# Performance work log

Hardware: AMD Instinct MI355X
Metric: run time of the kernel (lower is better)

## Reference

```python
import jax, jax.numpy as jnp
import numpy as np

D_MODEL = 32
D_STATE = 16
D_CONV = 4
D_INNER = 64  # expand * d_model
DT_RANK = 2   # ceil(d_model / 16)


def silu(x):
    return x * jax.nn.sigmoid(x)


def _mamba_params(key, scale=0.05):
    ks = jax.random.split(key, 7)
    p = {}
    p['in_w'] = jax.random.normal(ks[0], (2 * D_INNER, D_MODEL), jnp.float32) * scale
    p['conv_w'] = jax.random.normal(ks[1], (D_INNER, 1, D_CONV), jnp.float32) * scale
    p['conv_b'] = jax.random.normal(ks[2], (D_INNER,), jnp.float32) * scale
    p['xproj_w'] = jax.random.normal(ks[3], (DT_RANK + 2 * D_STATE, D_INNER), jnp.float32) * scale
    p['dt_w'] = jax.random.normal(ks[4], (D_INNER, DT_RANK), jnp.float32) * scale
    p['dt_b'] = jax.random.normal(ks[5], (D_INNER,), jnp.float32) * scale
    # S4D-real init: A = [1..d_state] broadcast over d_inner
    p['A_log'] = jnp.log(jnp.broadcast_to(jnp.arange(1, D_STATE + 1, dtype=jnp.float32), (D_INNER, D_STATE)))
    p['D'] = jnp.ones((D_INNER,), jnp.float32)
    p['out_w'] = jax.random.normal(ks[6], (D_MODEL, D_INNER), jnp.float32) * scale
    return p


def mamba(x, in_w, conv_w, conv_b, xproj_w, dt_w, dt_b, A_log, Dp, out_w):
    # x: (B, L, d_model)
    Bsz, L, _ = x.shape
    xz = x @ in_w.T                                   # (B, L, 2*d_inner)
    xi, z = jnp.split(xz, 2, axis=-1)
    # causal depthwise conv over L
    xc = jnp.pad(xi.transpose(0, 2, 1), ((0, 0), (0, 0), (D_CONV - 1, 0)))  # (B, d_inner, L+3)
    xc = jax.lax.conv_general_dilated(xc, conv_w, (1,), 'VALID',
                                      dimension_numbers=('NCH', 'OIH', 'NCH'),
                                      feature_group_count=D_INNER)
    xi = silu(xc.transpose(0, 2, 1) + conv_b)          # (B, L, d_inner)
    dbc = xi @ xproj_w.T                               # (B, L, dt_rank + 2*d_state)
    dt = dbc[..., :DT_RANK]
    Bm = dbc[..., DT_RANK:DT_RANK + D_STATE]           # (B, L, d_state)
    Cm = dbc[..., DT_RANK + D_STATE:]                  # (B, L, d_state)
    delta = jax.nn.softplus(dt @ dt_w.T + dt_b)        # (B, L, d_inner)
    A = -jnp.exp(A_log)                                # (d_inner, d_state)
    deltaA = jnp.exp(delta[..., None] * A)             # (B, L, d_inner, d_state)
    deltaBx = delta[..., None] * Bm[:, :, None, :] * xi[..., None]

    def step(h, t):
        dA, dBx = t
        h = dA * h + dBx
        return h, h

    h0 = jnp.zeros((Bsz, D_INNER, D_STATE), x.dtype)
    _, hs = jax.lax.scan(step, h0, (deltaA.transpose(1, 0, 2, 3), deltaBx.transpose(1, 0, 2, 3)))
    hs = hs.transpose(1, 0, 2, 3)                      # (B, L, d_inner, d_state)
    y = jnp.einsum('blds,bls->bld', hs, Cm) + Dp * xi
    y = y * silu(z)
    return y @ out_w.T                                 # (B, L, d_model)


def setup_inputs() -> dict:
    key = jax.random.key(0)
    ks = jax.random.split(key, 12)
    s = 0.05
    inp = {'inputs': jax.random.normal(ks[0], (32, 512, 64, 64), jnp.float32)}
    inp['proj_avg_w'] = jax.random.normal(ks[1], (D_MODEL, 1), jnp.float32) * s
    inp['proj_avg_b'] = jax.random.normal(ks[2], (D_MODEL,), jnp.float32) * s
    inp['proj_max_w'] = jax.random.normal(ks[3], (D_MODEL, 1), jnp.float32) * s
    inp['proj_max_b'] = jax.random.normal(ks[4], (D_MODEL,), jnp.float32) * s
    inp['gate_w'] = jax.random.normal(ks[5], (1, 2), jnp.float32) * s
    inp['gate_b'] = jax.random.normal(ks[6], (1,), jnp.float32) * s
    inp['out_w'] = jax.random.normal(ks[7], (1, D_MODEL), jnp.float32) * s
    inp['out_b'] = jax.random.normal(ks[8], (1,), jnp.float32) * s
    pf = _mamba_params(ks[9])
    pb = _mamba_params(ks[10])
    for k, v in pf.items():
        inp['f_' + k] = v
    for k, v in pb.items():
        inp['b_' + k] = v
    return inp


def reference(inputs, proj_avg_w, proj_avg_b, proj_max_w, proj_max_b, gate_w, gate_b,
              out_w, out_b,
              f_in_w, f_conv_w, f_conv_b, f_xproj_w, f_dt_w, f_dt_b, f_A_log, f_D, f_out_w,
              b_in_w, b_conv_w, b_conv_b, b_xproj_w, b_dt_w, b_dt_b, b_A_log, b_D, b_out_w):
    # global avg / max pool -> (B, C, 1)
    x_avg = jnp.mean(inputs, axis=(2, 3))[..., None]
    x_max = jnp.max(inputs, axis=(2, 3))[..., None]
    gate_in = jnp.concatenate([x_avg, x_max], axis=-1)            # (B, C, 2)
    alpha = jax.nn.sigmoid(gate_in @ gate_w.T + gate_b)           # (B, C, 1)
    xa = x_avg @ proj_avg_w.T + proj_avg_b                        # (B, C, d_model)
    xm = x_max @ proj_max_w.T + proj_max_b
    fwd = (f_in_w, f_conv_w, f_conv_b, f_xproj_w, f_dt_w, f_dt_b, f_A_log, f_D, f_out_w)
    bwd = (b_in_w, b_conv_w, b_conv_b, b_xproj_w, b_dt_w, b_dt_b, b_A_log, b_D, b_out_w)
    y_avg = mamba(xa, *fwd) + jnp.flip(mamba(jnp.flip(xa, 1), *bwd), 1)
    y_max = mamba(xm, *fwd) + jnp.flip(mamba(jnp.flip(xm, 1), *bwd), 1)
    y = alpha * y_avg + (1.0 - alpha) * y_max
    att = jax.nn.sigmoid(y @ out_w.T + out_b)                     # (B, C, 1)
    return att[..., None]                                         # (B, C, 1, 1)
```

## Files before the change

### kernel.cpp

```cpp
#include <hip/hip_runtime.h>
#include <math.h>

#define OFF_YPART 32768
#define OFF_PD    294912
#define OFF_PX    (OFF_PD + 4194304)
#define OFF_PG    (OFF_PX + 4194304)
#define OFF_BCB   (OFF_PG + 4194304)
#define OFF_BCC   (OFF_BCB + 524288)
#define OFF_YB    (OFF_BCC + 524288)

__global__ __launch_bounds__(256) void kreduce(const float* __restrict__ in,
                                               float* __restrict__ xavg,
                                               float* __restrict__ xmax) {
    const int bl = blockIdx.x;
    const float* p = in + (size_t)bl * 4096;
    const int t = threadIdx.x;
    float s = 0.f, m = -INFINITY;
#pragma unroll
    for (int it = 0; it < 4; ++it) {
        float4 v = *reinterpret_cast<const float4*>(p + (size_t)(it * 256 + t) * 4);
        s += v.x + v.y + v.z + v.w;
        m = fmaxf(m, fmaxf(fmaxf(v.x, v.y), fmaxf(v.z, v.w)));
    }
#pragma unroll
    for (int o = 1; o < 64; o <<= 1) {
        s += __shfl_xor(s, o);
        m = fmaxf(m, __shfl_xor(m, o));
    }
    __shared__ float ls[4], lm[4];
    const int w = t >> 6;
    if ((t & 63) == 0) { ls[w] = s; lm[w] = m; }
    __syncthreads();
    if (t == 0) {
        s = ls[0] + ls[1] + ls[2] + ls[3];
        m = fmaxf(fmaxf(lm[0], lm[1]), fmaxf(lm[2], lm[3]));
        xavg[bl] = s * (1.f / 4096.f);
        xmax[bl] = m;
    }
}

__device__ __forceinline__ int dbc_slot(int j) {
    return j < 2 ? j : (j < 18 ? 2 * j - 2 : 2 * j - 33);
}

__global__ __launch_bounds__(512) void kprep(
    const float* __restrict__ xavg, const float* __restrict__ xmax,
    float* __restrict__ ws,
    const float* __restrict__ paw, const float* __restrict__ pab,
    const float* __restrict__ pmw, const float* __restrict__ pmb,
    const float* __restrict__ outw_outer,
    const float* __restrict__ f_in_w, const float* __restrict__ f_conv_w,
    const float* __restrict__ f_conv_b, const float* __restrict__ f_xproj_w,
    const float* __restrict__ f_dt_w, const float* __restrict__ f_dt_b,
    const float* __restrict__ f_D, const float* __restrict__ f_out_w,
    const float* __restrict__ b_in_w, const float* __restrict__ b_conv_w,
    const float* __restrict__ b_conv_b, const float* __restrict__ b_xproj_w,
    const float* __restrict__ b_dt_w, const float* __restrict__ b_dt_b,
    const float* __restrict__ b_D, const float* __restrict__ b_out_w)
{
    const int tid = threadIdx.x;
    const int c  = blockIdx.x >> 8;
    const int b  = (blockIdx.x >> 3) & 31;
    const int cq = blockIdx.x & 7;
    const int strm = c >> 1, dir = c & 1;

    const float* in_w = dir ? b_in_w   : f_in_w;
    const float* cwp  = dir ? b_conv_w : f_conv_w;
    const float* cbp  = dir ? b_conv_b : f_conv_b;
    const float* xpw  = dir ? b_xproj_w: f_xproj_w;
    const float* dtwp = dir ? b_dt_w   : f_dt_w;
    const float* dtbp = dir ? b_dt_b   : f_dt_b;
    const float* Dpar = dir ? b_D      : f_D;
    const float* owp  = dir ? b_out_w  : f_out_w;
    const float* projw = strm ? pmw : paw;
    const float* projb = strm ? pmb : pab;
    const float* xin   = strm ? xmax : xavg;

    __shared__ float sseq4[68];
    __shared__ float su[128], sv[128];
    __shared__ float scw[64][4], scb[64], sdtw[64][2], sdtb[64], sD[64], swf[64];
    __shared__ float sxp[34][68];
    __shared__ float sxi[64][68];
    __shared__ float sdbc[64][37];

    if (tid < 67) {
        int g = cq * 64 - 3 + tid;
        float val = 0.f;
        if (g >= 0) val = xin[b * 512 + (dir ? (511 - g) : g)];
        sseq4[tid] = val;
    }
    if (tid < 128) {
        float u = 0.f, v = 0.f;
        const float* row = in_w + tid * 32;
#pragma unroll
        for (int m = 0; m < 32; ++m) {
            u = fmaf(row[m], projw[m], u);
            v = fmaf(row[m], projb[m], v);
        }
        su[tid] = u; sv[tid] = v;
    }
    if (tid < 64) {
#pragma unroll
        for (int k = 0; k < 4; ++k) scw[tid][k] = cwp[tid * 4 + k];
        scb[tid] = cbp[tid];
        sdtw[tid][0] = dtwp[tid * 2];
        sdtw[tid][1] = dtwp[tid * 2 + 1];
        sdtb[tid] = dtbp[tid];
        sD[tid] = Dpar[tid];
        float wf = 0.f;
#pragma unroll
        for (int m = 0; m < 32; ++m) wf = fmaf(outw_outer[m], owp[m * 64 + tid], wf);
        swf[tid] = wf;
    }
    for (int i = tid; i < 34 * 64; i += 512) sxp[i >> 6][i & 63] = xpw[i];
    __syncthreads();

    const int ll8 = tid >> 3;
    const int j8  = tid & 7;
    const int gi  = cq * 64 + ll8;

    {
        float t0 = sseq4[ll8], t1 = sseq4[ll8 + 1], t2 = sseq4[ll8 + 2], t3 = sseq4[ll8 + 3];
        float vv0 = (gi >= 3) ? 1.f : 0.f;
        float vv1 = (gi >= 2) ? 1.f : 0.f;
        float vv2 = (gi >= 1) ? 1.f : 0.f;
#pragma unroll
        for (int k = 0; k < 8; ++k) {
            int di = j8 * 8 + k;
            float u = su[di], v = sv[di];
            float xc = scw[di][0] * fmaf(t0, u, vv0 * v)
                     + scw[di][1] * fmaf(t1, u, vv1 * v)
                     + scw[di][2] * fmaf(t2, u, vv2 * v)
                     + scw[di][3] * fmaf(t3, u, v);
            xc += scb[di];
            float sig = 1.f / (1.f + __expf(-xc));
            sxi[ll8][di] = xc * sig;
        }
    }
    __syncthreads();

    {
        float a0 = 0.f, a1 = 0.f, a2 = 0.f, a3 = 0.f, a4 = 0.f;
        const float4* xr4 = reinterpret_cast<const float4*>(&sxi[ll8][0]);
        const float4* r0 = reinterpret_cast<const float4*>(&sxp[j8 + 0][0]);
        const float4* r1 = reinterpret_cast<const float4*>(&sxp[j8 + 8][0]);
        const float4* r2 = reinterpret_cast<const float4*>(&sxp[j8 + 16][0]);
        const float4* r3 = reinterpret_cast<const float4*>(&sxp[j8 + 24][0]);
        const float4* r4 = (j8 < 2) ? reinterpret_cast<const float4*>(&sxp[j8 + 32][0]) : r0;
        bool extra = (j8 < 2);
#pragma unroll 2
        for (int q = 0; q < 16; ++q) {
            float4 x = xr4[q];
            float4 w;
            w = r0[q]; a0 = fmaf(x.x,w.x,fmaf(x.y,w.y,fmaf(x.z,w.z,fmaf(x.w,w.w,a0))));
            w = r1[q]; a1 = fmaf(x.x,w.x,fmaf(x.y,w.y,fmaf(x.z,w.z,fmaf(x.w,w.w,a1))));
            w = r2[q]; a2 = fmaf(x.x,w.x,fmaf(x.y,w.y,fmaf(x.z,w.z,fmaf(x.w,w.w,a2))));
            w = r3[q]; a3 = fmaf(x.x,w.x,fmaf(x.y,w.y,fmaf(x.z,w.z,fmaf(x.w,w.w,a3))));
            if (extra) { w = r4[q]; a4 = fmaf(x.x,w.x,fmaf(x.y,w.y,fmaf(x.z,w.z,fmaf(x.w,w.w,a4)))); }
        }
        sdbc[ll8][dbc_slot(j8)]      = a0;
        sdbc[ll8][dbc_slot(j8 + 8)]  = a1;
        sdbc[ll8][dbc_slot(j8 + 16)] = a2;
        sdbc[ll8][dbc_slot(j8 + 24)] = a3;
        if (extra) sdbc[ll8][dbc_slot(j8 + 32)] = a4;
    }
    __syncthreads();

    {
        const size_t tile = ((size_t)(c * 32 + b) * 8 + cq) * 4096;
        float dt0 = sdbc[ll8][0], dt1 = sdbc[ll8][1];
        float x3 = sseq4[ll8 + 3];
        float ybp = 0.f;
#pragma unroll 2
        for (int k = 0; k < 8; ++k) {
            int di = j8 * 8 + k;
            float xi = sxi[ll8][di];
            float pre = fmaf(dt0, sdtw[di][0], fmaf(dt1, sdtw[di][1], sdtb[di]));
            float sp = (pre > 20.f) ? pre : __logf(1.f + __expf(pre));
            float zv = fmaf(x3, su[64 + di], sv[64 + di]);
            float g = (zv / (1.f + __expf(-zv))) * swf[di];
            ws[OFF_PD + tile + di * 64 + ll8] = sp;
            ws[OFF_PX + tile + di * 64 + ll8] = sp * xi;
            ws[OFF_PG + tile + di * 64 + ll8] = g;
            ybp = fmaf(g * sD[di], xi, ybp);
        }
        ybp += __shfl_xor(ybp, 1);
        ybp += __shfl_xor(ybp, 2);
        ybp += __shfl_xor(ybp, 4);
        if (j8 == 0) ws[OFF_YB + (size_t)(c * 32 + b) * 512 + gi] = ybp;
    }

    {
        const size_t bb = ((size_t)(c * 32 + b) * 8 + cq) * 1024;
        for (int i = tid; i < 1024; i += 512) {
            int s = i >> 6, t = i & 63;
            ws[OFF_BCB + bb + i] = sdbc[t][2 + 2 * s];
            ws[OFF_BCC + bb + i] = sdbc[t][3 + 2 * s];
        }
    }
}

#define DPP_ADD(v, ctrl) ((v) + __int_as_float(__builtin_amdgcn_update_dpp(0, __float_as_int(v), (ctrl), 0xF, 0xF, true)))

__global__ __launch_bounds__(256) void kscan(
    float* __restrict__ ws,
    const float* __restrict__ f_A_log, const float* __restrict__ b_A_log)
{
    const int tid = threadIdx.x;
    const int c  = blockIdx.x >> 7;
    const int dq = (blockIdx.x >> 5) & 3;
    const int b  = blockIdx.x & 31;
    const int dir = c & 1;
    const float* alog = dir ? b_A_log : f_A_log;

    const int dd = tid >> 4;
    const int s  = tid & 15;
    const int d  = dq * 16 + dd;
    const float cA = -expf(alog[d * 16 + s]) * 1.44269504088896340736f;
    float h = 0.f;

    __shared__ float sd[16][68], sx[16][68], sg[16][68];
    __shared__ float sB[16][68], sC[16][68];
    __shared__ float syT[16][68];
    __shared__ float syb[64];

    const int srow = tid >> 4;
    const int scol = (tid & 15) * 4;
    float* ypart = ws + OFF_YPART;
    const size_t cb512 = (size_t)(c * 32 + b) * 512;

    {
        const size_t tb = (size_t)(c * 32 + b) * 8;
        *reinterpret_cast<float4*>(&sd[srow][scol]) =
            *reinterpret_cast<const float4*>(ws + OFF_PD + tb * 4096 + dq * 1024 + srow * 64 + scol);
        *reinterpret_cast<float4*>(&sx[srow][scol]) =
            *reinterpret_cast<const float4*>(ws + OFF_PX + tb * 4096 + dq * 1024 + srow * 64 + scol);
        *reinterpret_cast<float4*>(&sg[srow][scol]) =
            *reinterpret_cast<const float4*>(ws + OFF_PG + tb * 4096 + dq * 1024 + srow * 64 + scol);
        *reinterpret_cast<float4*>(&sB[srow][scol]) =
            *reinterpret_cast<const float4*>(ws + OFF_BCB + tb * 1024 + srow * 64 + scol);
        *reinterpret_cast<float4*>(&sC[srow][scol]) =
            *reinterpret_cast<const float4*>(ws + OFF_BCC + tb * 1024 + srow * 64 + scol);
        if (dq == 0 && tid < 64) syb[tid] = ws[OFF_YB + cb512 + tid];
    }
    __syncthreads();

    for (int chunk = 0; chunk < 8; ++chunk) {
        float4 nd, nx, ng, nB, nC;
        float nyb = 0.f;
        const bool pf = (chunk < 7);
        if (pf) {
            const size_t tb1 = (size_t)(c * 32 + b) * 8 + chunk + 1;
            nd = *reinterpret_cast<const float4*>(ws + OFF_PD + tb1 * 4096 + dq * 1024 + srow * 64 + scol);
            nx = *reinterpret_cast<const float4*>(ws + OFF_PX + tb1 * 4096 + dq * 1024 + srow * 64 + scol);
            ng = *reinterpret_cast<const float4*>(ws + OFF_PG + tb1 * 4096 + dq * 1024 + srow * 64 + scol);
            nB = *reinterpret_cast<const float4*>(ws + OFF_BCB + tb1 * 1024 + srow * 64 + scol);
            nC = *reinterpret_cast<const float4*>(ws + OFF_BCC + tb1 * 1024 + srow * 64 + scol);
            if (dq == 0 && tid < 64) nyb = ws[OFF_YB + cb512 + (chunk + 1) * 64 + tid];
        }

        {
#pragma unroll 2
            for (int m = 0; m < 16; ++m) {
                float4 de = *reinterpret_cast<const float4*>(&sd[dd][4 * m]);
                float4 dx = *reinterpret_cast<const float4*>(&sx[dd][4 * m]);
                float4 gq = *reinterpret_cast<const float4*>(&sg[dd][4 * m]);
                float4 Bq = *reinterpret_cast<const float4*>(&sB[s][4 * m]);
                float4 Cq = *reinterpret_cast<const float4*>(&sC[s][4 * m]);
                float4 val;
                float a, pc;
                a = exp2f(de.x * cA); h = fmaf(a, h, dx.x * Bq.x); pc = h * Cq.x;
                pc = DPP_ADD(pc, 0x101); pc = DPP_ADD(pc, 0x102);
                pc = DPP_ADD(pc, 0x104); pc = DPP_ADD(pc, 0x108);
                val.x = pc * gq.x;
                a = exp2f(de.y * cA); h = fmaf(a, h, dx.y * Bq.y); pc = h * Cq.y;
                pc = DPP_ADD(pc, 0x101); pc = DPP_ADD(pc, 0x102);
                pc = DPP_ADD(pc, 0x104); pc = DPP_ADD(pc, 0x108);
                val.y = pc * gq.y;
                a = exp2f(de.z * cA); h = fmaf(a, h, dx.z * Bq.z); pc = h * Cq.z;
                pc = DPP_ADD(pc, 0x101); pc = DPP_ADD(pc, 0x102);
                pc = DPP_ADD(pc, 0x104); pc = DPP_ADD(pc, 0x108);
                val.z = pc * gq.z;
                a = exp2f(de.w * cA); h = fmaf(a, h, dx.w * Bq.w); pc = h * Cq.w;
                pc = DPP_ADD(pc, 0x101); pc = DPP_ADD(pc, 0x102);
                pc = DPP_ADD(pc, 0x104); pc = DPP_ADD(pc, 0x108);
                val.w = pc * gq.w;
                if (s == 0) *reinterpret_cast<float4*>(&syT[dd][4 * m]) = val;
            }
        }
        __syncthreads();

        {
            const int tt4 = tid >> 2;
            const int j4  = tid & 3;
            float acc = syT[j4 * 4][tt4] + syT[j4 * 4 + 1][tt4]
                      + syT[j4 * 4 + 2][tt4] + syT[j4 * 4 + 3][tt4];
            acc += __shfl_xor(acc, 1);
            acc += __shfl_xor(acc, 2);
            if (j4 == 0) {
                int i = chunk * 64 + tt4;
                int l = dir ? (511 - i) : i;
                float res = acc + (dq == 0 ? syb[tt4] : 0.f);
                ypart[((c * 4 + dq) * 32 + b) * 512 + l] = res;
            }
        }
        __syncthreads();

        if (pf) {
            *reinterpret_cast<float4*>(&sd[srow][scol]) = nd;
            *reinterpret_cast<float4*>(&sx[srow][scol]) = nx;
            *reinterpret_cast<float4*>(&sg[srow][scol]) = ng;
            *reinterpret_cast<float4*>(&sB[srow][scol]) = nB;
            *reinterpret_cast<float4*>(&sC[srow][scol]) = nC;
            if (dq == 0 && tid < 64) syb[tid] = nyb;
            __syncthreads();
        }
    }
}

__global__ __launch_bounds__(256) void kfinal(const float* __restrict__ xavg,
                                              const float* __restrict__ xmax,
                                              const float* __restrict__ ypart,
                                              const float* __restrict__ gate_w,
                                              const float* __restrict__ gate_b,
                                              const float* __restrict__ out_b,
                                              float* __restrict__ out) {
    const int idx = blockIdx.x * 256 + threadIdx.x;
    float xa = xavg[idx], xm = xmax[idx];
    float alpha = 1.f / (1.f + __expf(-(fmaf(xa, gate_w[0], fmaf(xm, gate_w[1], gate_b[0])))));
    float sa = 0.f, sm = 0.f;
#pragma unroll
    for (int k = 0; k < 8; ++k)  sa += ypart[k * 16384 + idx];
#pragma unroll
    for (int k = 8; k < 16; ++k) sm += ypart[k * 16384 + idx];
    float y = alpha * sa + (1.f - alpha) * sm + out_b[0];
    out[idx] = 1.f / (1.f + __expf(-y));
}

extern "C" void kernel_launch(void* const* d_in, const int* in_sizes, int n_in,
                              void* d_out, int out_size, void* d_ws, size_t ws_size,
                              hipStream_t stream) {
    const float* inp = (const float*)d_in[0];
    const float* paw = (const float*)d_in[1];
    const float* pab = (const float*)d_in[2];
    const float* pmw = (const float*)d_in[3];
    const float* pmb = (const float*)d_in[4];
    const float* gw  = (const float*)d_in[5];
    const float* gb  = (const float*)d_in[6];
    const float* ow  = (const float*)d_in[7];
    const float* ob  = (const float*)d_in[8];

    float* ws = (float*)d_ws;
    float* xavg = ws;
    float* xmax = ws + 16384;
    float* ypart = ws + OFF_YPART;
    float* out = (float*)d_out;

    kreduce<<<16384, 256, 0, stream>>>(inp, xavg, xmax);
    kprep<<<1024, 512, 0, stream>>>(
        xavg, xmax, ws, paw, pab, pmw, pmb, ow,
        (const float*)d_in[9],  (const float*)d_in[10], (const float*)d_in[11], (const float*)d_in[12],
        (const float*)d_in[13], (const float*)d_in[14], (const float*)d_in[16], (const float*)d_in[17],
        (const float*)d_in[18], (const float*)d_in[19], (const float*)d_in[20], (const float*)d_in[21],
        (const float*)d_in[22], (const float*)d_in[23], (const float*)d_in[25], (const float*)d_in[26]);
    kscan<<<512, 256, 0, stream>>>(
        ws, (const float*)d_in[15], (const float*)d_in[24]);
    kfinal<<<64, 256, 0, stream>>>(xavg, xmax, ypart, gw, gb, ob, out);
}
```

Before: 123.6 us.

## Double-buffer scan shared tiles and shorten DPP state reduction to four lanes

Shared-memory staging in the scan kernel becomes double-buffered, so the next chunk's prefetched values are written into the alternate buffer before the same barrier that ends the compute phase. This removes one __syncthreads per chunk. The 16-lane DPP reduction over state is cut to 4 lanes, and four partial sums per row are written to an enlarged syT buffer that the output phase sums across. This drops two DPP steps per timestep in exchange for more shared-memory writes and reads, and the larger LDS footprint may lower occupancy.

New measurement: 117.9 us. 4.6% less time.

```diff
diff --git a/kernel.cpp b/kernel.cpp
--- a/kernel.cpp
+++ b/kernel.cpp
@@ -219,10 +219,10 @@
     const float cA = -expf(alog[d * 16 + s]) * 1.44269504088896340736f;
     float h = 0.f;
 
-    __shared__ float sd[16][68], sx[16][68], sg[16][68];
-    __shared__ float sB[16][68], sC[16][68];
-    __shared__ float syT[16][68];
-    __shared__ float syb[64];
+    __shared__ float sd[2][16][68], sx[2][16][68], sg[2][16][68];
+    __shared__ float sB[2][16][68], sC[2][16][68];
+    __shared__ float syT[4][17][68];
+    __shared__ float syb[2][64];
 
     const int srow = tid >> 4;
     const int scol = (tid & 15) * 4;
@@ -231,21 +231,22 @@
 
     {
         const size_t tb = (size_t)(c * 32 + b) * 8;
-        *reinterpret_cast<float4*>(&sd[srow][scol]) =
+        *reinterpret_cast<float4*>(&sd[0][srow][scol]) =
             *reinterpret_cast<const float4*>(ws + OFF_PD + tb * 4096 + dq * 1024 + srow * 64 + scol);
-        *reinterpret_cast<float4*>(&sx[srow][scol]) =
+        *reinterpret_cast<float4*>(&sx[0][srow][scol]) =
             *reinterpret_cast<const float4*>(ws + OFF_PX + tb * 4096 + dq * 1024 + srow * 64 + scol);
-        *reinterpret_cast<float4*>(&sg[srow][scol]) =
+        *reinterpret_cast<float4*>(&sg[0][srow][scol]) =
             *reinterpret_cast<const float4*>(ws + OFF_PG + tb * 4096 + dq * 1024 + srow * 64 + scol);
-        *reinterpret_cast<float4*>(&sB[srow][scol]) =
+        *reinterpret_cast<float4*>(&sB[0][srow][scol]) =
             *reinterpret_cast<const float4*>(ws + OFF_BCB + tb * 1024 + srow * 64 + scol);
-        *reinterpret_cast<float4*>(&sC[srow][scol]) =
+        *reinterpret_cast<float4*>(&sC[0][srow][scol]) =
             *reinterpret_cast<const float4*>(ws + OFF_BCC + tb * 1024 + srow * 64 + scol);
-        if (dq == 0 && tid < 64) syb[tid] = ws[OFF_YB + cb512 + tid];
+        if (dq == 0 && tid < 64) syb[0][tid] = ws[OFF_YB + cb512 + tid];
     }
     __syncthreads();
 
     for (int chunk = 0; chunk < 8; ++chunk) {
+        const int cur = chunk & 1;
         float4 nd, nx, ng, nB, nC;
         float nyb = 0.f;
         const bool pf = (chunk < 7);
@@ -262,59 +263,60 @@
         {
 #pragma unroll 2
             for (int m = 0; m < 16; ++m) {
-                float4 de = *reinterpret_cast<const float4*>(&sd[dd][4 * m]);
-                float4 dx = *reinterpret_cast<const float4*>(&sx[dd][4 * m]);
-                float4 gq = *reinterpret_cast<const float4*>(&sg[dd][4 * m]);
-                float4 Bq = *reinterpret_cast<const float4*>(&sB[s][4 * m]);
-                float4 Cq = *reinterpret_cast<const float4*>(&sC[s][4 * m]);
+                float4 de = *reinterpret_cast<const float4*>(&sd[cur][dd][4 * m]);
+                float4 dx = *reinterpret_cast<const float4*>(&sx[cur][dd][4 * m]);
+                float4 gq = *reinterpret_cast<const float4*>(&sg[cur][dd][4 * m]);
+                float4 Bq = *reinterpret_cast<const float4*>(&sB[cur][s][4 * m]);
+                float4 Cq = *reinterpret_cast<const float4*>(&sC[cur][s][4 * m]);
                 float4 val;
                 float a, pc;
                 a = exp2f(de.x * cA); h = fmaf(a, h, dx.x * Bq.x); pc = h * Cq.x;
                 pc = DPP_ADD(pc, 0x101); pc = DPP_ADD(pc, 0x102);
-                pc = DPP_ADD(pc, 0x104); pc = DPP_ADD(pc, 0x108);
                 val.x = pc * gq.x;
                 a = exp2f(de.y * cA); h = fmaf(a, h, dx.y * Bq.y); pc = h * Cq.y;
                 pc = DPP_ADD(pc, 0x101); pc = DPP_ADD(pc, 0x102);
-                pc = DPP_ADD(pc, 0x104); pc = DPP_ADD(pc, 0x108);
                 val.y = pc * gq.y;
                 a = exp2f(de.z * cA); h = fmaf(a, h, dx.z * Bq.z); pc = h * Cq.z;
                 pc = DPP_ADD(pc, 0x101); pc = DPP_ADD(pc, 0x102);
-                pc = DPP_ADD(pc, 0x104); pc = DPP_ADD(pc, 0x108);
                 val.z = pc * gq.z;
                 a = exp2f(de.w * cA); h = fmaf(a, h, dx.w * Bq.w); pc = h * Cq.w;
                 pc = DPP_ADD(pc, 0x101); pc = DPP_ADD(pc, 0x102);
-                pc = DPP_ADD(pc, 0x104); pc = DPP_ADD(pc, 0x108);
                 val.w = pc * gq.w;
-                if (s == 0) *reinterpret_cast<float4*>(&syT[dd][4 * m]) = val;
+                if ((s & 3) == 0) *reinterpret_cast<float4*>(&syT[s >> 2][dd][4 * m]) = val;
             }
+        }
+
+        if (pf) {
+            *reinterpret_cast<float4*>(&sd[cur ^ 1][srow][scol]) = nd;
+            *reinterpret_cast<float4*>(&sx[cur ^ 1][srow][scol]) = nx;
+            *reinterpret_cast<float4*>(&sg[cur ^ 1][srow][scol]) = ng;
+            *reinterpret_cast<float4*>(&sB[cur ^ 1][srow][scol]) = nB;
+            *reinterpret_cast<float4*>(&sC[cur ^ 1][srow][scol]) = nC;
+            if (dq == 0 && tid < 64) syb[cur ^ 1][tid] = nyb;
         }
         __syncthreads();
 
         {
             const int tt4 = tid >> 2;
             const int j4  = tid & 3;
-            float acc = syT[j4 * 4][tt4] + syT[j4 * 4 + 1][tt4]
-                      + syT[j4 * 4 + 2][tt4] + syT[j4 * 4 + 3][tt4];
+            float acc = 0.f;
+#pragma unroll
+            for (int sg4 = 0; sg4 < 4; ++sg4) {
+#pragma unroll
+                for (int k = 0; k < 4; ++k) {
+                    acc += syT[sg4][j4 * 4 + k][tt4];
+                }
+            }
             acc += __shfl_xor(acc, 1);
             acc += __shfl_xor(acc, 2);
             if (j4 == 0) {
                 int i = chunk * 64 + tt4;
                 int l = dir ? (511 - i) : i;
-                float res = acc + (dq == 0 ? syb[tt4] : 0.f);
+                float res = acc + (dq == 0 ? syb[cur][tt4] : 0.f);
                 ypart[((c * 4 + dq) * 32 + b) * 512 + l] = res;
             }
         }
         __syncthreads();
-
-        if (pf) {
-            *reinterpret_cast<float4*>(&sd[srow][scol]) = nd;
-            *reinterpret_cast<float4*>(&sx[srow][scol]) = nx;
-            *reinterpret_cast<float4*>(&sg[srow][scol]) = ng;
-            *reinterpret_cast<float4*>(&sB[srow][scol]) = nB;
-            *reinterpret_cast<float4*>(&sC[srow][scol]) = nC;
-            if (dq == 0 && tid < 64) syb[tid] = nyb;
-            __syncthreads();
-        }
     }
 }
 
```
